# Kernel tuning notes

Measured on AMD Instinct MI355X. Metric: run time of the kernel, lower is better.

The kernel has to match this reference:

```python
import jax, jax.numpy as jnp
import numpy as np

DIM = 1024

def setup_inputs() -> dict:
    key = jax.random.key(0)
    k1, k2, k3, k4 = jax.random.split(key, 4)
    B, L, D = 32, 2048, DIM
    x = jax.random.normal(k1, (B, D), dtype=jnp.float32)
    context = jax.random.normal(k2, (B, L, D), dtype=jnp.float32)
    # linear_concatWa: Linear(2*dim, dim, bias=False) -> weight [dim, 2*dim]
    Wa = jax.random.normal(k3, (D, 2 * D), dtype=jnp.float32) * (1.0 / np.sqrt(2 * D))
    # linear_concatVa: Linear(dim, 1, bias=False) -> weight [1, dim]
    Va = jax.random.normal(k4, (1, D), dtype=jnp.float32) * (1.0 / np.sqrt(D))
    return {"x": x, "context": context, "Wa": Wa, "Va": Va}


def reference(x, context, Wa, Va):
    # concat-mode additive (Bahdanau) attention.
    # Wa @ cat(ht, hs) == ht @ Wa[:, :D].T + hs @ Wa[:, D:].T  (avoids materializing concat)
    D = x.shape[-1]
    Wa_t, Wa_s = Wa[:, :D], Wa[:, D:]              # each [D, D]
    ht_proj = jnp.einsum('bd,kd->bk', x, Wa_t)     # [B, D]
    hs_proj = jnp.einsum('bld,kd->blk', context, Wa_s)  # [B, L, D]
    hidden = jnp.tanh(ht_proj[:, None, :] + hs_proj)    # [B, L, D]
    scores = jnp.einsum('blk,ok->bl', hidden, Va)       # [B, L]  (Va: [1, D])
    attn = jax.nn.softmax(scores, axis=-1)               # [B, L]
    weighted = jnp.einsum('bl,bld->bd', attn, context)   # [B, D]
    return weighted, attn
```

## Files before the change

### kernel.cpp

```cpp
#include <hip/hip_runtime.h>
#include <hip/hip_bf16.h>
#include <cstdint>
#include <cstddef>

#define DIM 1024
#define B_SZ 32
#define L_SZ 2048

#define BM 128
#define BN 128

typedef __attribute__((ext_vector_type(8))) short bf16x8;
typedef __attribute__((ext_vector_type(4))) float floatx4;

static __device__ __forceinline__ unsigned cvt2_bf16_rne(float a, float b) {
    unsigned ua = __builtin_bit_cast(unsigned, a);
    unsigned ub = __builtin_bit_cast(unsigned, b);
    ua = (ua + 0x7FFFu + ((ua >> 16) & 1u)) >> 16;
    ub = (ub + 0x7FFFu + ((ub >> 16) & 1u)) >> 16;
    return ua | (ub << 16);
}

static __device__ __forceinline__ float bf2f(unsigned short u) {
    return __builtin_bit_cast(float, (unsigned)u << 16);
}

static __device__ __forceinline__ float tanh_fast(float x) {
    float e = __expf(2.0f * x);
    return 1.0f - 2.0f * __builtin_amdgcn_rcpf(e + 1.0f);
}

static __device__ __forceinline__ void gld_lds16(const void* g, void* lds) {
    __builtin_amdgcn_global_load_lds(
        (const __attribute__((address_space(1))) unsigned int*)g,
        (__attribute__((address_space(3))) unsigned int*)lds,
        16, 0, 0);
}

__global__ __launch_bounds__(256) void cvt_ctx_kernel(const float* __restrict__ src,
                                                      unsigned short* __restrict__ dst,
                                                      long n8) {
    long i = (long)blockIdx.x * 256 + threadIdx.x;
    const long stride = (long)gridDim.x * 256;
    for (; i < n8; i += stride) {
        const float4 a = ((const float4*)src)[i * 2];
        const float4 b = ((const float4*)src)[i * 2 + 1];
        uint4 o;
        o.x = cvt2_bf16_rne(a.x, a.y);
        o.y = cvt2_bf16_rne(a.z, a.w);
        o.z = cvt2_bf16_rne(b.x, b.y);
        o.w = cvt2_bf16_rne(b.z, b.w);
        ((uint4*)dst)[i] = o;
    }
}

__global__ __launch_bounds__(256) void cvt_wa_kernel(const float* __restrict__ Wa,
                                                     unsigned short* __restrict__ dst) {
    const int i = blockIdx.x * 256 + threadIdx.x;
    const int k = i >> 7, dc = i & 127;
    const float* s = Wa + (size_t)k * (2 * DIM) + DIM + dc * 8;
    const float4 a = ((const float4*)s)[0];
    const float4 b = ((const float4*)s)[1];
    uint4 o;
    o.x = cvt2_bf16_rne(a.x, a.y);
    o.y = cvt2_bf16_rne(a.z, a.w);
    o.z = cvt2_bf16_rne(b.x, b.y);
    o.w = cvt2_bf16_rne(b.z, b.w);
    ((uint4*)(dst + (size_t)k * DIM + dc * 8))[0] = o;
}

__global__ __launch_bounds__(256) void ht_kernel(const float* __restrict__ x,
                                                 const float* __restrict__ Wa,
                                                 float* __restrict__ ht) {
    const int b = blockIdx.x, kb = blockIdx.y, t = threadIdx.x;
    __shared__ float xs[DIM];
    for (int i = t; i < DIM; i += 256) xs[i] = x[b * DIM + i];
    __syncthreads();
    const int wave = t >> 6, lane = t & 63;
    for (int kk = 0; kk < 16; ++kk) {
        const int k = kb * 64 + wave * 16 + kk;
        const float* wr = Wa + (size_t)k * (2 * DIM);
        float s = 0.f;
        #pragma unroll
        for (int d = 0; d < DIM; d += 64) s += xs[d + lane] * wr[d + lane];
        #pragma unroll
        for (int off = 32; off > 0; off >>= 1) s += __shfl_xor(s, off);
        if (lane == 0) ht[b * DIM + k] = s;
    }
}

__global__ __launch_bounds__(256) void gemm_score_bf16(
    const unsigned short* __restrict__ A, const unsigned short* __restrict__ Bm,
    const float* __restrict__ Va, const float* __restrict__ ht,
    float* __restrict__ scores)
{
    __shared__ __align__(16) unsigned short As[BM * 64];
    __shared__ __align__(16) unsigned short Bs[BN * 64];
    const int t = threadIdx.x;
    const int n0 = blockIdx.x * BN;
    const int m0 = blockIdx.y * BM;
    const int lane = t & 63, wave = t >> 6;
    const int l15 = lane & 15, quad = lane >> 4;
    const int wm = (wave >> 1) * 64, wn = (wave & 1) * 64;

    const int lr = lane >> 3;
    const int lc = (lane & 7) ^ lr;
    const size_t aRow = (size_t)(m0 + wave * 32 + lr);
    const size_t bRow = (size_t)(n0 + wave * 32 + lr);

    floatx4 acc[4][4];
    #pragma unroll
    for (int i = 0; i < 4; ++i)
        #pragma unroll
        for (int j = 0; j < 4; ++j) acc[i][j] = (floatx4)0.f;

    for (int k0 = 0; k0 < DIM; k0 += 64) {
        #pragma unroll
        for (int q = 0; q < 4; ++q) {
            gld_lds16(A + (aRow + q * 8) * DIM + k0 + lc * 8,
                      &As[(wave * 32 + q * 8) * 64]);
            gld_lds16(Bm + (bRow + q * 8) * DIM + k0 + lc * 8,
                      &Bs[(wave * 32 + q * 8) * 64]);
        }
        __syncthreads();

        bf16x8 af[2][4], bv[2][4];
        #pragma unroll
        for (int kb = 0; kb < 2; ++kb) {
            #pragma unroll
            for (int i = 0; i < 4; ++i) {
                const int r = wm + i * 16 + l15;
                const int c = (kb * 4 + quad) ^ (r & 7);
                af[kb][i] = *(const bf16x8*)&As[r * 64 + c * 8];
            }
            #pragma unroll
            for (int j = 0; j < 4; ++j) {
                const int r = wn + j * 16 + l15;
                const int c = (kb * 4 + quad) ^ (r & 7);
                bv[kb][j] = *(const bf16x8*)&Bs[r * 64 + c * 8];
            }
        }
        #pragma unroll
        for (int kb = 0; kb < 2; ++kb)
            #pragma unroll
            for (int i = 0; i < 4; ++i)
                #pragma unroll
                for (int j = 0; j < 4; ++j)
                    acc[i][j] = __builtin_amdgcn_mfma_f32_16x16x32_bf16(
                        af[kb][i], bv[kb][j], acc[i][j], 0, 0, 0);
        __syncthreads();
    }

    const int bb = m0 >> 11;
    float htv[4], vav[4];
    #pragma unroll
    for (int j = 0; j < 4; ++j) {
        const int ng = n0 + wn + j * 16 + l15;
        htv[j] = ht[bb * DIM + ng];
        vav[j] = Va[ng];
    }
    #pragma unroll
    for (int i = 0; i < 4; ++i) {
        #pragma unroll
        for (int r = 0; r < 4; ++r) {
            float s = 0.f;
            #pragma unroll
            for (int j = 0; j < 4; ++j)
                s += tanh_fast(acc[i][j][r] + htv[j]) * vav[j];
            s += __shfl_xor(s, 8);
            s += __shfl_xor(s, 4);
            s += __shfl_xor(s, 2);
            s += __shfl_xor(s, 1);
            if (l15 == 0)
                atomicAdd(&scores[m0 + wm + i * 16 + quad * 4 + r], s);
        }
    }
}

#define LDS_STRIDE 40
__global__ __launch_bounds__(256, 2) void gemm_score_kernel(
    const float* __restrict__ ctx, const float* __restrict__ Wa,
    const float* __restrict__ Va, const float* __restrict__ ht,
    float* __restrict__ scores)
{
    __shared__ unsigned short As[BM * LDS_STRIDE];
    __shared__ unsigned short Bs[BN * LDS_STRIDE];
    const int t = threadIdx.x;
    const int n0 = blockIdx.x * BN;
    const int m0 = blockIdx.y * BM;
    const int lane = t & 63, wave = t >> 6;
    const int l15 = lane & 15, quad = lane >> 4;
    const int wm = (wave >> 1) * 64, wn = (wave & 1) * 64;
    const int srow = t >> 3;
    const int scol = (t & 7) * 4;
    const float* aBase = ctx + (size_t)(m0 + srow) * DIM + scol;
    const float* bBase = Wa + (size_t)(n0 + srow) * (2 * DIM) + DIM + scol;

    floatx4 acc[4][4];
    #pragma unroll
    for (int i = 0; i < 4; ++i)
        #pragma unroll
        for (int j = 0; j < 4; ++j) acc[i][j] = (floatx4)0.f;

    for (int k0 = 0; k0 < DIM; k0 += 32) {
        __syncthreads();
        #pragma unroll
        for (int r = 0; r < 4; ++r) {
            const float4 va = *(const float4*)(aBase + (size_t)(r * 32) * DIM + k0);
            const float4 vb = *(const float4*)(bBase + (size_t)(r * 32) * (2 * DIM) + k0);
            *(uint2*)&As[(srow + r * 32) * LDS_STRIDE + scol] =
                make_uint2(cvt2_bf16_rne(va.x, va.y), cvt2_bf16_rne(va.z, va.w));
            *(uint2*)&Bs[(srow + r * 32) * LDS_STRIDE + scol] =
                make_uint2(cvt2_bf16_rne(vb.x, vb.y), cvt2_bf16_rne(vb.z, vb.w));
        }
        __syncthreads();
        bf16x8 af[4], bfr[4];
        #pragma unroll
        for (int i = 0; i < 4; ++i)
            af[i] = *(const bf16x8*)&As[(wm + i * 16 + l15) * LDS_STRIDE + quad * 8];
        #pragma unroll
        for (int j = 0; j < 4; ++j)
            bfr[j] = *(const bf16x8*)&Bs[(wn + j * 16 + l15) * LDS_STRIDE + quad * 8];
        #pragma unroll
        for (int i = 0; i < 4; ++i)
            #pragma unroll
            for (int j = 0; j < 4; ++j)
                acc[i][j] = __builtin_amdgcn_mfma_f32_16x16x32_bf16(af[i], bfr[j], acc[i][j], 0, 0, 0);
    }
    const int bb = m0 >> 11;
    float htv[4], vav[4];
    #pragma unroll
    for (int j = 0; j < 4; ++j) {
        const int ng = n0 + wn + j * 16 + l15;
        htv[j] = ht[bb * DIM + ng];
        vav[j] = Va[ng];
    }
    #pragma unroll
    for (int i = 0; i < 4; ++i) {
        #pragma unroll
        for (int r = 0; r < 4; ++r) {
            float s = 0.f;
            #pragma unroll
            for (int j = 0; j < 4; ++j)
                s += tanh_fast(acc[i][j][r] + htv[j]) * vav[j];
            s += __shfl_xor(s, 8);
            s += __shfl_xor(s, 4);
            s += __shfl_xor(s, 2);
            s += __shfl_xor(s, 1);
            if (l15 == 0)
                atomicAdd(&scores[m0 + wm + i * 16 + quad * 4 + r], s);
        }
    }
}

__global__ __launch_bounds__(256) void softmax_kernel(const float* __restrict__ scores,
                                                      float* __restrict__ attn) {
    const int b = blockIdx.x, t = threadIdx.x;
    const float* sc = scores + b * L_SZ;
    float* at = attn + b * L_SZ;
    __shared__ float red[256];
    float m = -1e30f;
    for (int l = t; l < L_SZ; l += 256) m = fmaxf(m, sc[l]);
    red[t] = m; __syncthreads();
    for (int s = 128; s > 0; s >>= 1) { if (t < s) red[t] = fmaxf(red[t], red[t + s]); __syncthreads(); }
    m = red[0]; __syncthreads();
    float sum = 0.f;
    for (int l = t; l < L_SZ; l += 256) sum += __expf(sc[l] - m);
    red[t] = sum; __syncthreads();
    for (int s = 128; s > 0; s >>= 1) { if (t < s) red[t] += red[t + s]; __syncthreads(); }
    const float inv = 1.0f / red[0];
    for (int l = t; l < L_SZ; l += 256) at[l] = __expf(sc[l] - m) * inv;
}

__global__ __launch_bounds__(128) void weighted_bf16_kernel(
    const unsigned short* __restrict__ ctxb, const float* __restrict__ attn,
    float* __restrict__ weighted) {
    const int b = blockIdx.x, slice = blockIdx.y, t = threadIdx.x;
    const unsigned short* cb = ctxb + ((size_t)b * L_SZ + (size_t)slice * 128) * DIM + t * 8;
    const float* at = attn + b * L_SZ + slice * 128;
    float acc[8] = {0.f, 0.f, 0.f, 0.f, 0.f, 0.f, 0.f, 0.f};
    for (int l = 0; l < 128; ++l) {
        const float a = at[l];
        const uint4 v = *(const uint4*)(cb + (size_t)l * DIM);
        const unsigned w0 = v.x, w1 = v.y, w2 = v.z, w3 = v.w;
        acc[0] += a * bf2f((unsigned short)(w0 & 0xFFFF));
        acc[1] += a * bf2f((unsigned short)(w0 >> 16));
        acc[2] += a * bf2f((unsigned short)(w1 & 0xFFFF));
        acc[3] += a * bf2f((unsigned short)(w1 >> 16));
        acc[4] += a * bf2f((unsigned short)(w2 & 0xFFFF));
        acc[5] += a * bf2f((unsigned short)(w2 >> 16));
        acc[6] += a * bf2f((unsigned short)(w3 & 0xFFFF));
        acc[7] += a * bf2f((unsigned short)(w3 >> 16));
    }
    float* o = weighted + b * DIM + t * 8;
    #pragma unroll
    for (int e = 0; e < 8; ++e) atomicAdd(o + e, acc[e]);
}

__global__ __launch_bounds__(256) void weighted_kernel(const float* __restrict__ ctx,
                                                       const float* __restrict__ attn,
                                                       float* __restrict__ weighted) {
    const int b = blockIdx.x, slice = blockIdx.y, t = threadIdx.x;
    const float* cb = ctx + ((size_t)b * L_SZ + (size_t)slice * 128) * DIM;
    const float* at = attn + b * L_SZ + slice * 128;
    float4 w = make_float4(0.f, 0.f, 0.f, 0.f);
    for (int l = 0; l < 128; ++l) {
        const float a = at[l];
        const float4 c = *(const float4*)(cb + (size_t)l * DIM + t * 4);
        w.x += a * c.x; w.y += a * c.y; w.z += a * c.z; w.w += a * c.w;
    }
    float* o = weighted + b * DIM + t * 4;
    atomicAdd(o + 0, w.x);
    atomicAdd(o + 1, w.y);
    atomicAdd(o + 2, w.z);
    atomicAdd(o + 3, w.w);
}

extern "C" void kernel_launch(void* const* d_in, const int* in_sizes, int n_in,
                              void* d_out, int out_size, void* d_ws, size_t ws_size,
                              hipStream_t stream) {
    const float* x   = (const float*)d_in[0];
    const float* ctx = (const float*)d_in[1];
    const float* Wa  = (const float*)d_in[2];
    const float* Va  = (const float*)d_in[3];

    float* out      = (float*)d_out;
    float* weighted = out;
    float* attn     = out + B_SZ * DIM;

    float* scores = (float*)d_ws;
    float* ht     = scores + B_SZ * L_SZ;

    const size_t base = (size_t)(B_SZ * L_SZ + B_SZ * DIM) * sizeof(float);
    const size_t need = base + (size_t)DIM * DIM * 2
                      + (size_t)B_SZ * L_SZ * DIM * 2;

    hipMemsetAsync(scores, 0, (size_t)B_SZ * L_SZ * sizeof(float), stream);
    hipMemsetAsync(weighted, 0, (size_t)B_SZ * DIM * sizeof(float), stream);

    ht_kernel<<<dim3(B_SZ, 16), 256, 0, stream>>>(x, Wa, ht);

    if (ws_size >= need) {
        unsigned short* WaB  = (unsigned short*)((char*)d_ws + base);
        unsigned short* ctxB = WaB + (size_t)DIM * DIM;
        cvt_wa_kernel<<<512, 256, 0, stream>>>(Wa, WaB);
        cvt_ctx_kernel<<<8192, 256, 0, stream>>>(ctx, ctxB,
                                                 (long)B_SZ * L_SZ * DIM / 8);
        gemm_score_bf16<<<dim3(DIM / BN, (B_SZ * L_SZ) / BM), 256, 0, stream>>>(
            ctxB, WaB, Va, ht, scores);
        softmax_kernel<<<B_SZ, 256, 0, stream>>>(scores, attn);
        weighted_bf16_kernel<<<dim3(B_SZ, 16), 128, 0, stream>>>(ctxB, attn, weighted);
    } else {
        gemm_score_kernel<<<dim3(DIM / BN, (B_SZ * L_SZ) / BM), 256, 0, stream>>>(
            ctx, Wa, Va, ht, scores);
        softmax_kernel<<<B_SZ, 256, 0, stream>>>(scores, attn);
        weighted_kernel<<<dim3(B_SZ, 16), 256, 0, stream>>>(ctx, attn, weighted);
    }
}
```

Baseline: 616.2 us.

## Fuse preprocessing kernels and memsets into one launch; fuse softmax into weighted sum

Merges the context bf16 conversion, Wa conversion, ht projection and the two zero-fills into a single pre_kernel, with each role selected by block-index range. The softmax is fused into the weighted-sum kernel: each slice block recomputes the row max and sum and writes its own attn slice. This removes several launches and memset calls plus the attn round trip. In exchange, every one of the 16 slice blocks per batch row re-reads the full score row, and the context conversion now uses narrower 8-byte stores.

```diff
diff --git a/kernel.cpp b/kernel.cpp
--- a/kernel.cpp
+++ b/kernel.cpp
@@ -9,6 +9,10 @@
 
 #define BM 128
 #define BN 128
+
+#define CVT_BLOCKS 8192
+#define HT_BLOCKS  512
+#define WA_BLOCKS  512
 
 typedef __attribute__((ext_vector_type(8))) short bf16x8;
 typedef __attribute__((ext_vector_type(4))) float floatx4;
@@ -21,8 +25,8 @@
     return ua | (ub << 16);
 }
 
-static __device__ __forceinline__ float bf2f(unsigned short u) {
-    return __builtin_bit_cast(float, (unsigned)u << 16);
+static __device__ __forceinline__ float bf2f(unsigned u16) {
+    return __builtin_bit_cast(float, u16 << 16);
 }
 
 static __device__ __forceinline__ float tanh_fast(float x) {
@@ -37,55 +41,61 @@
         16, 0, 0);
 }
 
-__global__ __launch_bounds__(256) void cvt_ctx_kernel(const float* __restrict__ src,
-                                                      unsigned short* __restrict__ dst,
-                                                      long n8) {
-    long i = (long)blockIdx.x * 256 + threadIdx.x;
-    const long stride = (long)gridDim.x * 256;
-    for (; i < n8; i += stride) {
-        const float4 a = ((const float4*)src)[i * 2];
-        const float4 b = ((const float4*)src)[i * 2 + 1];
+__global__ __launch_bounds__(256) void pre_kernel(
+    const float* __restrict__ x, const float* __restrict__ ctx,
+    const float* __restrict__ Wa,
+    unsigned short* __restrict__ ctxB, unsigned short* __restrict__ WaB,
+    float* __restrict__ ht, float* __restrict__ scores,
+    float* __restrict__ weighted)
+{
+    const int bid = blockIdx.x, t = threadIdx.x;
+
+    if (bid < CVT_BLOCKS) {
+        const long n4 = (long)B_SZ * L_SZ * DIM / 4;
+        const long stride = (long)CVT_BLOCKS * 256;
+        for (long i = (long)bid * 256 + t; i < n4; i += stride) {
+            const float4 a = ((const float4*)ctx)[i];
+            ((uint2*)ctxB)[i] =
+                make_uint2(cvt2_bf16_rne(a.x, a.y), cvt2_bf16_rne(a.z, a.w));
+        }
+    } else if (bid < CVT_BLOCKS + HT_BLOCKS) {
+        const int lb = bid - CVT_BLOCKS;
+        const int gi = lb * 256 + t;
+        if (gi < B_SZ * L_SZ) scores[gi] = 0.f;
+        const int b = lb >> 4, kb = lb & 15;
+        __shared__ float xs[DIM];
+        for (int i = t; i < DIM; i += 256) xs[i] = x[b * DIM + i];
+        __syncthreads();
+        const int wave = t >> 6, lane = t & 63;
+        const float4* xs4 = (const float4*)xs;
+        for (int kk = 0; kk < 16; ++kk) {
+            const int k = kb * 64 + wave * 16 + kk;
+            const float4* wr = (const float4*)(Wa + (size_t)k * (2 * DIM));
+            float s = 0.f;
+            #pragma unroll
+            for (int d = 0; d < DIM / 4; d += 64) {
+                const float4 w4 = wr[d + lane];
+                const float4 x4 = xs4[d + lane];
+                s += w4.x * x4.x + w4.y * x4.y + w4.z * x4.z + w4.w * x4.w;
+            }
+            #pragma unroll
+            for (int off = 32; off > 0; off >>= 1) s += __shfl_xor(s, off);
+            if (lane == 0) ht[b * DIM + k] = s;
+        }
+    } else {
+        const int lb = bid - CVT_BLOCKS - HT_BLOCKS;
+        const int i = lb * 256 + t;
+        if (i < B_SZ * DIM) weighted[i] = 0.f;
+        const int k = i >> 7, dc = i & 127;
+        const float* s = Wa + (size_t)k * (2 * DIM) + DIM + dc * 8;
+        const float4 a = ((const float4*)s)[0];
+        const float4 b4 = ((const float4*)s)[1];
         uint4 o;
         o.x = cvt2_bf16_rne(a.x, a.y);
         o.y = cvt2_bf16_rne(a.z, a.w);
-        o.z = cvt2_bf16_rne(b.x, b.y);
-        o.w = cvt2_bf16_rne(b.z, b.w);
-        ((uint4*)dst)[i] = o;
-    }
-}
-
-__global__ __launch_bounds__(256) void cvt_wa_kernel(const float* __restrict__ Wa,
-                                                     unsigned short* __restrict__ dst) {
-    const int i = blockIdx.x * 256 + threadIdx.x;
-    const int k = i >> 7, dc = i & 127;
-    const float* s = Wa + (size_t)k * (2 * DIM) + DIM + dc * 8;
-    const float4 a = ((const float4*)s)[0];
-    const float4 b = ((const float4*)s)[1];
-    uint4 o;
-    o.x = cvt2_bf16_rne(a.x, a.y);
-    o.y = cvt2_bf16_rne(a.z, a.w);
-    o.z = cvt2_bf16_rne(b.x, b.y);
-    o.w = cvt2_bf16_rne(b.z, b.w);
-    ((uint4*)(dst + (size_t)k * DIM + dc * 8))[0] = o;
-}
-
-__global__ __launch_bounds__(256) void ht_kernel(const float* __restrict__ x,
-                                                 const float* __restrict__ Wa,
-                                                 float* __restrict__ ht) {
-    const int b = blockIdx.x, kb = blockIdx.y, t = threadIdx.x;
-    __shared__ float xs[DIM];
-    for (int i = t; i < DIM; i += 256) xs[i] = x[b * DIM + i];
-    __syncthreads();
-    const int wave = t >> 6, lane = t & 63;
-    for (int kk = 0; kk < 16; ++kk) {
-        const int k = kb * 64 + wave * 16 + kk;
-        const float* wr = Wa + (size_t)k * (2 * DIM);
-        float s = 0.f;
-        #pragma unroll
-        for (int d = 0; d < DIM; d += 64) s += xs[d + lane] * wr[d + lane];
-        #pragma unroll
-        for (int off = 32; off > 0; off >>= 1) s += __shfl_xor(s, off);
-        if (lane == 0) ht[b * DIM + k] = s;
+        o.z = cvt2_bf16_rne(b4.x, b4.y);
+        o.w = cvt2_bf16_rne(b4.z, b4.w);
+        ((uint4*)(WaB + (size_t)k * DIM + dc * 8))[0] = o;
     }
 }
 
@@ -177,7 +187,75 @@
     }
 }
 
+__global__ __launch_bounds__(256) void post_kernel(
+    const float* __restrict__ scores, const unsigned short* __restrict__ ctxB,
+    float* __restrict__ attn, float* __restrict__ weighted)
+{
+    const int b = blockIdx.x, slice = blockIdx.y, t = threadIdx.x;
+    const float* sc = scores + b * L_SZ;
+    __shared__ float red[256];
+    __shared__ float att[128];
+
+    float m = -1e30f;
+    for (int l = t; l < L_SZ; l += 256) m = fmaxf(m, sc[l]);
+    red[t] = m; __syncthreads();
+    for (int s = 128; s > 0; s >>= 1) { if (t < s) red[t] = fmaxf(red[t], red[t + s]); __syncthreads(); }
+    m = red[0]; __syncthreads();
+    float sum = 0.f;
+    for (int l = t; l < L_SZ; l += 256) sum += __expf(sc[l] - m);
+    red[t] = sum; __syncthreads();
+    for (int s = 128; s > 0; s >>= 1) { if (t < s) red[t] += red[t + s]; __syncthreads(); }
+    const float inv = 1.0f / red[0];
+
+    const int l0 = slice * 128;
+    if (t < 128) {
+        const float av = __expf(sc[l0 + t] - m) * inv;
+        att[t] = av;
+        attn[b * L_SZ + l0 + t] = av;
+    }
+    __syncthreads();
+
+    const unsigned short* cb = ctxB + ((size_t)b * L_SZ + l0) * DIM + t * 4;
+    float a0 = 0.f, a1 = 0.f, a2 = 0.f, a3 = 0.f;
+    for (int l = 0; l < 128; ++l) {
+        const float a = att[l];
+        const uint2 v = *(const uint2*)(cb + (size_t)l * DIM);
+        a0 += a * bf2f(v.x & 0xFFFFu);
+        a1 += a * bf2f(v.x >> 16);
+        a2 += a * bf2f(v.y & 0xFFFFu);
+        a3 += a * bf2f(v.y >> 16);
+    }
+    float* o = weighted + b * DIM + t * 4;
+    atomicAdd(o + 0, a0);
+    atomicAdd(o + 1, a1);
+    atomicAdd(o + 2, a2);
+    atomicAdd(o + 3, a3);
+}
+
 #define LDS_STRIDE 40
+__global__ __launch_bounds__(256) void ht_kernel_fb(const float* __restrict__ x,
+                                                    const float* __restrict__ Wa,
+                                                    float* __restrict__ ht,
+                                                    float* __restrict__ scores) {
+    const int b = blockIdx.x, kb = blockIdx.y, t = threadIdx.x;
+    const int gidx = (b * 16 + kb) * 256 + t;
+    if (gidx < B_SZ * L_SZ) scores[gidx] = 0.f;
+    __shared__ float xs[DIM];
+    for (int i = t; i < DIM; i += 256) xs[i] = x[b * DIM + i];
+    __syncthreads();
+    const int wave = t >> 6, lane = t & 63;
+    for (int kk = 0; kk < 16; ++kk) {
+        const int k = kb * 64 + wave * 16 + kk;
+        const float* wr = Wa + (size_t)k * (2 * DIM);
+        float s = 0.f;
+        #pragma unroll
+        for (int d = 0; d < DIM; d += 64) s += xs[d + lane] * wr[d + lane];
+        #pragma unroll
+        for (int off = 32; off > 0; off >>= 1) s += __shfl_xor(s, off);
+        if (lane == 0) ht[b * DIM + k] = s;
+    }
+}
+
 __global__ __launch_bounds__(256, 2) void gemm_score_kernel(
     const float* __restrict__ ctx, const float* __restrict__ Wa,
     const float* __restrict__ Va, const float* __restrict__ ht,
@@ -253,12 +331,14 @@
     }
 }
 
-__global__ __launch_bounds__(256) void softmax_kernel(const float* __restrict__ scores,
-                                                      float* __restrict__ attn) {
-    const int b = blockIdx.x, t = threadIdx.x;
+__global__ __launch_bounds__(256) void post_kernel_fb(
+    const float* __restrict__ scores, const float* __restrict__ ctx,
+    float* __restrict__ attn, float* __restrict__ weighted)
+{
+    const int b = blockIdx.x, slice = blockIdx.y, t = threadIdx.x;
     const float* sc = scores + b * L_SZ;
-    float* at = attn + b * L_SZ;
     __shared__ float red[256];
+    __shared__ float att[128];
     float m = -1e30f;
     for (int l = t; l < L_SZ; l += 256) m = fmaxf(m, sc[l]);
     red[t] = m; __syncthreads();
@@ -269,44 +349,18 @@
     red[t] = sum; __syncthreads();
     for (int s = 128; s > 0; s >>= 1) { if (t < s) red[t] += red[t + s]; __syncthreads(); }
     const float inv = 1.0f / red[0];
-    for (int l = t; l < L_SZ; l += 256) at[l] = __expf(sc[l] - m) * inv;
-}
-
-__global__ __launch_bounds__(128) void weighted_bf16_kernel(
-    const unsigned short* __restrict__ ctxb, const float* __restrict__ attn,
-    float* __restrict__ weighted) {
-    const int b = blockIdx.x, slice = blockIdx.y, t = threadIdx.x;
-    const unsigned short* cb = ctxb + ((size_t)b * L_SZ + (size_t)slice * 128) * DIM + t * 8;
-    const float* at = attn + b * L_SZ + slice * 128;
-    float acc[8] = {0.f, 0.f, 0.f, 0.f, 0.f, 0.f, 0.f, 0.f};
-    for (int l = 0; l < 128; ++l) {
-        const float a = at[l];
-        const uint4 v = *(const uint4*)(cb + (size_t)l * DIM);
-        const unsigned w0 = v.x, w1 = v.y, w2 = v.z, w3 = v.w;
-        acc[0] += a * bf2f((unsigned short)(w0 & 0xFFFF));
-        acc[1] += a * bf2f((unsigned short)(w0 >> 16));
-        acc[2] += a * bf2f((unsigned short)(w1 & 0xFFFF));
-        acc[3] += a * bf2f((unsigned short)(w1 >> 16));
-        acc[4] += a * bf2f((unsigned short)(w2 & 0xFFFF));
-        acc[5] += a * bf2f((unsigned short)(w2 >> 16));
-        acc[6] += a * bf2f((unsigned short)(w3 & 0xFFFF));
-        acc[7] += a * bf2f((unsigned short)(w3 >> 16));
-    }
-    float* o = weighted + b * DIM + t * 8;
-    #pragma unroll
-    for (int e = 0; e < 8; ++e) atomicAdd(o + e, acc[e]);
-}
-
-__global__ __launch_bounds__(256) void weighted_kernel(const float* __restrict__ ctx,
-                                                       const float* __restrict__ attn,
-                                                       float* __restrict__ weighted) {
-    const int b = blockIdx.x, slice = blockIdx.y, t = threadIdx.x;
-    const float* cb = ctx + ((size_t)b * L_SZ + (size_t)slice * 128) * DIM;
-    const float* at = attn + b * L_SZ + slice * 128;
+    const int l0 = slice * 128;
+    if (t < 128) {
+        const float av = __expf(sc[l0 + t] - m) * inv;
+        att[t] = av;
+        attn[b * L_SZ + l0 + t] = av;
+    }
+    __syncthreads();
+    const float* cb = ctx + ((size_t)b * L_SZ + l0) * DIM + t * 4;
     float4 w = make_float4(0.f, 0.f, 0.f, 0.f);
     for (int l = 0; l < 128; ++l) {
-        const float a = at[l];
-        const float4 c = *(const float4*)(cb + (size_t)l * DIM + t * 4);
+        const float a = att[l];
+        const float4 c = *(const float4*)(cb + (size_t)l * DIM);
         w.x += a * c.x; w.y += a * c.y; w.z += a * c.z; w.w += a * c.w;
     }
     float* o = weighted + b * DIM + t * 4;
@@ -314,6 +368,11 @@
     atomicAdd(o + 1, w.y);
     atomicAdd(o + 2, w.z);
     atomicAdd(o + 3, w.w);
+}
+
+__global__ __launch_bounds__(256) void zero_weighted_fb(float* __restrict__ weighted) {
+    const int i = blockIdx.x * 256 + threadIdx.x;
+    if (i < B_SZ * DIM) weighted[i] = 0.f;
 }
 
 extern "C" void kernel_launch(void* const* d_in, const int* in_sizes, int n_in,
@@ -335,25 +394,19 @@
     const size_t need = base + (size_t)DIM * DIM * 2
                       + (size_t)B_SZ * L_SZ * DIM * 2;
 
-    hipMemsetAsync(scores, 0, (size_t)B_SZ * L_SZ * sizeof(float), stream);
-    hipMemsetAsync(weighted, 0, (size_t)B_SZ * DIM * sizeof(float), stream);
-
-    ht_kernel<<<dim3(B_SZ, 16), 256, 0, stream>>>(x, Wa, ht);
-
     if (ws_size >= need) {
         unsigned short* WaB  = (unsigned short*)((char*)d_ws + base);
         unsigned short* ctxB = WaB + (size_t)DIM * DIM;
-        cvt_wa_kernel<<<512, 256, 0, stream>>>(Wa, WaB);
-        cvt_ctx_kernel<<<8192, 256, 0, stream>>>(ctx, ctxB,
-                                                 (long)B_SZ * L_SZ * DIM / 8);
+        pre_kernel<<<CVT_BLOCKS + HT_BLOCKS + WA_BLOCKS, 256, 0, stream>>>(
+            x, ctx, Wa, ctxB, WaB, ht, scores, weighted);
         gemm_score_bf16<<<dim3(DIM / BN, (B_SZ * L_SZ) / BM), 256, 0, stream>>>(
             ctxB, WaB, Va, ht, scores);
-        softmax_kernel<<<B_SZ, 256, 0, stream>>>(scores, attn);
-        weighted_bf16_kernel<<<dim3(B_SZ, 16), 128, 0, stream>>>(ctxB, attn, weighted);
+        post_kernel<<<dim3(B_SZ, 16), 256, 0, stream>>>(scores, ctxB, attn, weighted);
     } else {
+        ht_kernel_fb<<<dim3(B_SZ, 16), 256, 0, stream>>>(x, Wa, ht, scores);
+        zero_weighted_fb<<<(B_SZ * DIM + 255) / 256, 256, 0, stream>>>(weighted);
         gemm_score_kernel<<<dim3(DIM / BN, (B_SZ * L_SZ) / BM), 256, 0, stream>>>(
             ctx, Wa, Va, ht, scores);
-        softmax_kernel<<<B_SZ, 256, 0, stream>>>(scores, attn);
-        weighted_kernel<<<dim3(B_SZ, 16), 256, 0, stream>>>(ctx, attn, weighted);
-    }
-}
+        post_kernel_fb<<<dim3(B_SZ, 16), 256, 0, stream>>>(scores, ctx, attn, weighted);
+    }
+}
```

Measured after the change: 603.3 us. 2.1% less time.
